# Performance work log

Hardware: AMD Instinct MI355X
Metric: run time of the kernel (lower is better)

Reference implementation:

```python
import jax, jax.numpy as jnp
import numpy as np

# ---- hardcoded module constants (from Cyborg.__init__) ----
B, S, V = 256, 128, 512
H = 30              # number of symbol vectors
N_STACKS = 2
R = 2               # REDUNDANCY
DEPTH = 4           # stack_depth
ZERO_OFFSET = 1e-6
NAND_BIAS = 3.0
INIT_SHARPEN = 10.0
N_VECS = 1 + N_STACKS  # input vec + one peek per stack = 3
C_BIG = (H + N_STACKS) * R   # 64 choices for push_fn / calc_out
C_SMALL = 2 * R              # 4 choices for pop_op / push_op


def _cossim(a, b, eps=1e-8):
    # torch.cosine_similarity semantics: per-vector norm clamp
    na = jnp.maximum(jnp.linalg.norm(a, axis=-1, keepdims=True), eps)
    nb = jnp.maximum(jnp.linalg.norm(b, axis=-1, keepdims=True), eps)
    return jnp.sum((a / na) * (b / nb), axis=-1)


def _nand(query, w, nw_raw):
    # Fuzzy-NAND gate bank (neurallambda NAND, clip='abs').
    # query: [B, N_VECS*V], w: [C, N_VECS*V], nw_raw: [C, N_VECS] -> [B, C]
    C = w.shape[0]
    q = query.reshape(-1, 1, N_VECS, V)
    wv = w.reshape(1, C, N_VECS, V)
    cos = jnp.abs(_cossim(q, wv))                 # [B, C, N_VECS], clip='abs'
    nw = jax.nn.sigmoid(nw_raw)[None]             # interpolate sim vs NOT(sim)
    interp = nw * cos + (1.0 - nw) * (1.0 - cos)
    return jnp.prod(interp, axis=-1)              # fuzzy AND over the 3 vecs


# ---- differentiable stack (soft pointer over DEPTH slots) ----
def _read(stack, ptr):
    return jnp.einsum('bdv,bd->bv', stack, ptr)

def _push(stack, ptr, val):
    p = jnp.roll(ptr, 1, axis=1)
    s = stack * (1.0 - p)[..., None] + val[:, None, :] * p[..., None]
    return s, p

def _pop(stack, ptr):
    s = stack * (1.0 - ptr)[..., None] + ZERO_OFFSET * ptr[..., None]
    p = jnp.roll(ptr, -1, axis=1)
    return s, p

def _pop_or_nop(stack, ptr, sharp, should_pop, should_nop):
    pr = jax.nn.softmax(jnp.stack([should_pop, should_nop], -1) * sharp, axis=-1)
    ps, pp = _pop(stack, ptr)
    s = ps * pr[:, 0, None, None] + stack * pr[:, 1, None, None]
    p = pp * pr[:, 0, None] + ptr * pr[:, 1, None]
    return s, p

def _push_or_nop(stack, ptr, sharp, should_push, should_nop, val):
    pr = jax.nn.softmax(jnp.stack([should_push, should_nop], -1) * sharp, axis=-1)
    ps, pp = _push(stack, ptr, val)
    s = ps * pr[:, 0, None, None] + stack * pr[:, 1, None, None]
    p = pp * pr[:, 0, None] + ptr * pr[:, 1, None]
    return s, p


def _forward(x, syms, stack_init_vec, sharp, pop_w, pop_nw, pushop_w, pushop_nw,
             pushfn_w, pushfn_nw, calc_w, calc_nw):
    b = x.shape[0]
    # init both stacks to zero_offset, pointer at slot 0, then hard-push init vec
    stack0 = jnp.full((N_STACKS, b, DEPTH, V), ZERO_OFFSET, x.dtype)
    ptr0 = jnp.zeros((N_STACKS, b, DEPTH), x.dtype).at[:, :, 0].set(1.0)
    init_val = jnp.broadcast_to(stack_init_vec, (b, V))
    stack0, ptr0 = jax.vmap(_push, in_axes=(0, 0, None))(stack0, ptr0, init_val)

    syms_b = jnp.broadcast_to(syms, (b, H, V))

    def step(carry, inp):
        stacks, ptrs = carry                                    # [2,B,D,V], [2,B,D]
        peeks = jax.vmap(_read)(stacks, ptrs)                   # [2,B,V]
        inps = jnp.concatenate([inp, peeks[0], peeks[1]], -1)   # [B,3V]
        out_opts = jnp.concatenate(
            [syms_b, peeks[0][:, None], peeks[1][:, None]], 1)  # [B,H+2,V]
        new_s, new_p = [], []
        for k in range(N_STACKS):
            pops = _nand(inps, pop_w[k], pop_nw[k])             # [B, 2R]
            pushes = _nand(inps, pushop_w[k], pushop_nw[k])     # [B, 2R]
            pv = _nand(inps, pushfn_w[k], pushfn_nw[k]).reshape(b, H + N_STACKS, R)
            push_val = jnp.einsum('bcv,bcr->bv', out_opts, pv)
            s, p = _pop_or_nop(stacks[k], ptrs[k], sharp[k],
                               pops[:, :R].max(1), pops[:, R:].max(1))
            s, p = _push_or_nop(s, p, sharp[k],
                                pushes[:, :R].max(1), pushes[:, R:].max(1), push_val)
            new_s.append(s)
            new_p.append(p)
        stacks = jnp.stack(new_s)
        ptrs = jnp.stack(new_p)
        peeks2 = jax.vmap(_read)(stacks, ptrs)
        inps2 = jnp.concatenate([inp, peeks2[0], peeks2[1]], -1)
        out_opts2 = jnp.concatenate(
            [syms_b, peeks2[0][:, None], peeks2[1][:, None]], 1)
        cv = _nand(inps2, calc_w, calc_nw).reshape(b, H + N_STACKS, R)
        out = jnp.einsum('bcv,bcr->bv', out_opts2, cv)
        return (stacks, ptrs), out

    _, outs = jax.lax.scan(step, (stack0, ptr0), jnp.swapaxes(x, 0, 1))
    return jnp.swapaxes(outs, 0, 1)  # [B,S,V]


def setup_inputs() -> dict:
    key = jax.random.key(0)
    ks = jax.random.split(key, 12)
    siv = jax.random.normal(ks[1], (V,), jnp.float32)
    siv = siv / jnp.linalg.norm(siv)
    return {
        'x': jax.random.normal(ks[0], (B, S, V), jnp.float32),
        'syms': jax.random.normal(ks[2], (H, V), jnp.float32),
        'stack_init_vec': siv,
        'sharp': jnp.full((N_STACKS,), INIT_SHARPEN, jnp.float32),
        'pop_w': jax.random.normal(ks[3], (N_STACKS, C_SMALL, N_VECS * V), jnp.float32),
        'pop_nw': jax.random.normal(ks[4], (N_STACKS, C_SMALL, N_VECS), jnp.float32) + NAND_BIAS,
        'pushop_w': jax.random.normal(ks[5], (N_STACKS, C_SMALL, N_VECS * V), jnp.float32),
        'pushop_nw': jax.random.normal(ks[6], (N_STACKS, C_SMALL, N_VECS), jnp.float32) + NAND_BIAS,
        'pushfn_w': jax.random.normal(ks[7], (N_STACKS, C_BIG, N_VECS * V), jnp.float32),
        'pushfn_nw': jax.random.normal(ks[8], (N_STACKS, C_BIG, N_VECS), jnp.float32) + NAND_BIAS,
        'calc_w': jax.random.normal(ks[9], (C_BIG, N_VECS * V), jnp.float32),
        'calc_nw': jax.random.normal(ks[10], (C_BIG, N_VECS), jnp.float32) + NAND_BIAS,
    }


def reference(x, syms, stack_init_vec, sharp, pop_w, pop_nw, pushop_w, pushop_nw,
              pushfn_w, pushfn_nw, calc_w, calc_nw):
    return _forward(x, syms, stack_init_vec, sharp, pop_w, pop_nw, pushop_w,
                    pushop_nw, pushfn_w, pushfn_nw, calc_w, calc_nw)
```

## Files before the change

kernel.cpp:

```cpp
#include <hip/hip_runtime.h>
#include <math.h>


#define SS 128
#define VV 512
#define NROWS 208
#define ZOFF 1e-6f

#define OFF_I0   0
#define OFF_OC   (32768*208)
#define OFF_GI   (OFF_OC + 32768*32)
#define OFF_M    (OFF_GI + 2*32*208)
#define OFF_A    (OFF_M + 1024)
#define OFF_Bc   (OFF_A + 624)
#define OFF_W0   (OFF_Bc + 624)

typedef _Float16 half8 __attribute__((ext_vector_type(8)));
typedef float f32x4 __attribute__((ext_vector_type(4)));

__device__ __forceinline__ const float* w_row(int r, const float* pw, const float* pow_,
                                              const float* pfw, const float* cw) {
    if (r < 8)   return pw   + r * 1536;
    if (r < 16)  return pow_ + (r - 8) * 1536;
    if (r < 144) return pfw  + (r - 16) * 1536;
    return cw + (r - 144) * 1536;
}
__device__ __forceinline__ const float* nw_row(int r, const float* pn, const float* pon,
                                               const float* pfn, const float* cn) {
    if (r < 8)   return pn   + r * 3;
    if (r < 16)  return pon  + (r - 8) * 3;
    if (r < 144) return pfn  + (r - 16) * 3;
    return cn + (r - 144) * 3;
}

__global__ void kB(const float* __restrict__ syms, const float* __restrict__ siv,
                   const float* __restrict__ pw, const float* __restrict__ pn,
                   const float* __restrict__ pow_, const float* __restrict__ pon,
                   const float* __restrict__ pfw, const float* __restrict__ pfn,
                   const float* __restrict__ cw, const float* __restrict__ cn,
                   float* __restrict__ ws) {
    int blk = blockIdx.x, tid = threadIdx.x;
    if (blk < 64) {
        int jj = blk >> 5, e = blk & 31;
        __shared__ float bas[512];
        for (int i = tid; i < 512; i += 256)
            bas[i] = (e == 0) ? 1.0f : ((e == 1) ? siv[i] : syms[(e - 2) * 512 + i]);
        __syncthreads();
        if (tid < NROWS) {
            int c = tid;
            const float4* w4 = (const float4*)(w_row(c, pw, pow_, pfw, cw) + (jj + 1) * 512);
            const float4* b4 = (const float4*)bas;
            float s = 0.f;
            for (int q = 0; q < 128; ++q) {
                float4 a = b4[q], b = w4[q];
                s += a.x * b.x + a.y * b.y + a.z * b.z + a.w * b.w;
            }
            ws[OFF_GI + (jj * 32 + e) * 208 + c] = s;
        }
    } else if (blk == 64) {
        __shared__ float basw[32 * 512];
        for (int i = tid; i < 32 * 512; i += 256) {
            int m = i >> 9, v = i & 511;
            basw[i] = (m == 0) ? 1.0f : ((m == 1) ? siv[v] : syms[(m - 2) * 512 + v]);
        }
        __syncthreads();
        for (int p = tid; p < 1024; p += 256) {
            int m = p >> 5, mm = p & 31;
            const float4* a4 = (const float4*)(basw + m * 512);
            const float4* b4 = (const float4*)(basw + mm * 512);
            float s = 0.f;
            for (int q = 0; q < 128; ++q) {
                float4 a = a4[q], b = b4[q];
                s += a.x * b.x + a.y * b.y + a.z * b.z + a.w * b.w;
            }
            ws[OFF_M + p] = s;
        }
    } else if (blk == 65) {
        for (int idx = tid; idx < 624; idx += 256) {
            int r = idx / 3, j = idx % 3;
            const float4* w4 = (const float4*)(w_row(r, pw, pow_, pfw, cw) + j * 512);
            float s = 0.f;
            for (int q = 0; q < 128; ++q) {
                float4 b = w4[q];
                s += b.x * b.x + b.y * b.y + b.z * b.z + b.w * b.w;
            }
            float nrm = fmaxf(sqrtf(s), 1e-8f);
            float nwv = nw_row(r, pn, pon, pfn, cn)[j];
            float sig = 1.f / (1.f + expf(-nwv));
            ws[OFF_A + idx]  = (2.f * sig - 1.f) / nrm;
            ws[OFF_Bc + idx] = 1.f - sig;
        }
    } else {
        int part = blk - 66;
        _Float16* whp = (_Float16*)(ws + OFF_W0);
        _Float16* wlp = whp + 208 * 512;
        for (int i = tid; i < 6656; i += 256) {
            int flat = part * 6656 + i;
            int c = flat >> 9, v = flat & 511;
            float wv = w_row(c, pw, pow_, pfw, cw)[v];
            _Float16 h = (_Float16)wv;
            whp[flat] = h;
            wlp[flat] = (_Float16)(wv - (float)h);
        }
    }
}

__global__ __launch_bounds__(256) void kA(const float* __restrict__ x, float* __restrict__ ws) {
    __shared__ half8 AH[2][256];
    __shared__ half8 AL[2][256];
    __shared__ float red[256];
    __shared__ float invx[64];
    const int tid = threadIdx.x;
    const int wid = tid >> 6, l = tid & 63;
    const size_t bt0 = (size_t)blockIdx.x * 64;

    const int sr = tid >> 2, ss = tid & 3;
    const float* xp = x + (bt0 + sr) * 512 + ss * 8;
    const int wpos = (sr >> 4) * 64 + (sr & 15) + (ss << 4);

    const _Float16* whp = (const _Float16*)(ws + OFF_W0);
    const _Float16* wlp = whp + 208 * 512;

    const int t0 = (wid == 0) ? 0 : (1 + 3 * wid);
    const int nt = (wid == 0) ? 4 : 3;

    f32x4 acc[4][4];
#pragma unroll
    for (int m = 0; m < 4; ++m)
#pragma unroll
        for (int tt = 0; tt < 4; ++tt)
            acc[m][tt] = (f32x4){0.f, 0.f, 0.f, 0.f};

    float sumsq = 0.f;
    auto stage = [&](int kt, int buf) {
        float v[8];
        *(float4*)v       = *(const float4*)(xp + kt * 32);
        *(float4*)(v + 4) = *(const float4*)(xp + kt * 32 + 4);
        half8 hh, hl;
#pragma unroll
        for (int j = 0; j < 8; ++j) {
            sumsq += v[j] * v[j];
            _Float16 h = (_Float16)v[j];
            hh[j] = h;
            hl[j] = (_Float16)(v[j] - (float)h);
        }
        AH[buf][wpos] = hh;
        AL[buf][wpos] = hl;
    };

    stage(0, 0);
    __syncthreads();

    for (int kt = 0; kt < 16; ++kt) {
        const int buf = kt & 1;
        if (kt < 15) stage(kt + 1, buf ^ 1);

        half8 ahm[4], alm[4];
#pragma unroll
        for (int m = 0; m < 4; ++m) {
            ahm[m] = AH[buf][m * 64 + l];
            alm[m] = AL[buf][m * 64 + l];
        }
        const int kof = kt * 32 + (l >> 4) * 8;
#pragma unroll
        for (int tt = 0; tt < 4; ++tt) {
            if (tt < nt) {
                const int c = (t0 + tt) * 16 + (l & 15);
                half8 bh = *(const half8*)(whp + c * 512 + kof);
                half8 bl = *(const half8*)(wlp + c * 512 + kof);
#pragma unroll
                for (int m = 0; m < 4; ++m) {
                    acc[m][tt] = __builtin_amdgcn_mfma_f32_16x16x32_f16(ahm[m], bh, acc[m][tt], 0, 0, 0);
                    acc[m][tt] = __builtin_amdgcn_mfma_f32_16x16x32_f16(ahm[m], bl, acc[m][tt], 0, 0, 0);
                    acc[m][tt] = __builtin_amdgcn_mfma_f32_16x16x32_f16(alm[m], bh, acc[m][tt], 0, 0, 0);
                }
            }
        }
        __syncthreads();
    }

    red[tid] = sumsq;
    __syncthreads();
    if (tid < 64) {
        float s = red[tid * 4] + red[tid * 4 + 1] + red[tid * 4 + 2] + red[tid * 4 + 3];
        invx[tid] = 1.f / fmaxf(sqrtf(s), 1e-8f);
    }
    __syncthreads();

#pragma unroll
    for (int tt = 0; tt < 4; ++tt) {
        if (tt < nt) {
            const int c = (t0 + tt) * 16 + (l & 15);
            const float A0 = ws[OFF_A + c * 3];
            const float B0 = ws[OFF_Bc + c * 3];
#pragma unroll
            for (int m = 0; m < 4; ++m) {
                const int rbase = m * 16 + (l >> 4) * 4;
#pragma unroll
                for (int j = 0; j < 4; ++j) {
                    const float ix = invx[rbase + j];
                    ws[OFF_I0 + (bt0 + rbase + j) * 208 + c] = A0 * fabsf(acc[m][tt][j]) * ix + B0;
                }
            }
        }
    }
}

__global__ __attribute__((amdgpu_flat_work_group_size(256, 256), amdgpu_waves_per_eu(1, 1)))
void kC(float* __restrict__ ws, const float* __restrict__ sharp) {
    __shared__ float pkL[64];
    __shared__ float nndL[144];
    const int b = blockIdx.x, tid = threadIdx.x;
    const int wid = tid >> 6, l = tid & 63;
    const int k = l >> 5, m = l & 31;
    const int isRow = (tid < 144);
    const int r2 = 144 + l;

    const float* GI = ws + OFF_GI;
    float G1[64], G2[64];
    float4 Mr[8];
    float A1r = 0.f, A2r = 0.f, B1r = 0.f, B2r = 0.f;
    float A1d = 0.f, A2d = 0.f, B1d = 0.f, B2d = 0.f;
    if (isRow) {
#pragma unroll
        for (int i = 0; i < 32; ++i) {
            G1[i]      = GI[i * 208 + tid];
            G1[32 + i] = GI[(32 + i) * 208 + tid];
        }
        A1r = ws[OFF_A + tid * 3 + 1];  A2r = ws[OFF_A + tid * 3 + 2];
        B1r = ws[OFF_Bc + tid * 3 + 1]; B2r = ws[OFF_Bc + tid * 3 + 2];
    }
    if (wid == 3) {
#pragma unroll
        for (int i = 0; i < 32; ++i) {
            G2[i]      = GI[i * 208 + r2];
            G2[32 + i] = GI[(32 + i) * 208 + r2];
        }
        A1d = ws[OFF_A + r2 * 3 + 1];  A2d = ws[OFF_A + r2 * 3 + 2];
        B1d = ws[OFF_Bc + r2 * 3 + 1]; B2d = ws[OFF_Bc + r2 * 3 + 2];
    }
#pragma unroll
    for (int q = 0; q < 8; ++q) Mr[q] = *(const float4*)(ws + OFF_M + m * 32 + q * 4);

    const float sh = sharp[k];

    float st[4], p[4];
#pragma unroll
    for (int d = 0; d < 4; ++d) {
        st[d] = (d == 1) ? ((m == 1) ? 1.f : 0.f) : ((m == 0) ? ZOFF : 0.f);
        p[d] = (d == 1) ? 1.f : 0.f;
    }
    float pk = st[0] * p[0] + st[1] * p[1] + st[2] * p[2] + st[3] * p[3];

    const float* i0base = ws + OFF_I0 + (size_t)b * SS * 208;
    float i0r  = isRow ? i0base[tid] : 0.f;
    float i0rn = 0.f;
    float i0d  = (wid == 3) ? i0base[r2] : 0.f;

    float iq0 = 1.f, iq1 = 1.f;
    auto gram_iq = [&](float own) {
        const float* ph = pkL + 32 * k;
        float4 a0 = *(const float4*)(ph);
        float4 a1 = *(const float4*)(ph + 4);
        float4 a2 = *(const float4*)(ph + 8);
        float4 a3 = *(const float4*)(ph + 12);
        float4 a4 = *(const float4*)(ph + 16);
        float4 a5 = *(const float4*)(ph + 20);
        float4 a6 = *(const float4*)(ph + 24);
        float4 a7 = *(const float4*)(ph + 28);
        float mva = Mr[0].x*a0.x + Mr[0].y*a0.y + Mr[0].z*a0.z + Mr[0].w*a0.w
                  + Mr[2].x*a2.x + Mr[2].y*a2.y + Mr[2].z*a2.z + Mr[2].w*a2.w
                  + Mr[4].x*a4.x + Mr[4].y*a4.y + Mr[4].z*a4.z + Mr[4].w*a4.w
                  + Mr[6].x*a6.x + Mr[6].y*a6.y + Mr[6].z*a6.z + Mr[6].w*a6.w;
        float mvb = Mr[1].x*a1.x + Mr[1].y*a1.y + Mr[1].z*a1.z + Mr[1].w*a1.w
                  + Mr[3].x*a3.x + Mr[3].y*a3.y + Mr[3].z*a3.z + Mr[3].w*a3.w
                  + Mr[5].x*a5.x + Mr[5].y*a5.y + Mr[5].z*a5.z + Mr[5].w*a5.w
                  + Mr[7].x*a7.x + Mr[7].y*a7.y + Mr[7].z*a7.z + Mr[7].w*a7.w;
        float part = own * (mva + mvb);
        part += __shfl_xor(part, 1);  part += __shfl_xor(part, 2);
        part += __shfl_xor(part, 4);  part += __shfl_xor(part, 8);
        part += __shfl_xor(part, 16);
        float iqOwn = 1.f / fmaxf(sqrtf(part), 1e-8f);
        float iqOth = __shfl_xor(iqOwn, 32);
        iq0 = k ? iqOth : iqOwn;
        iq1 = k ? iqOwn : iqOth;
    };
    auto dots = [&](const float* Gt, float& d1, float& d2) {
        float d1a = 0.f, d1b = 0.f, d2a = 0.f, d2b = 0.f;
#pragma unroll
        for (int q = 0; q < 8; q += 2) {
            float4 a = *(const float4*)(pkL + 4 * q);
            float4 bq = *(const float4*)(pkL + 4 * q + 4);
            float4 c = *(const float4*)(pkL + 32 + 4 * q);
            float4 e = *(const float4*)(pkL + 32 + 4 * q + 4);
            d1a += a.x * Gt[4*q]   + a.y * Gt[4*q+1]   + a.z * Gt[4*q+2]   + a.w * Gt[4*q+3];
            d1b += bq.x * Gt[4*q+4] + bq.y * Gt[4*q+5] + bq.z * Gt[4*q+6] + bq.w * Gt[4*q+7];
            d2a += c.x * Gt[32+4*q] + c.y * Gt[33+4*q] + c.z * Gt[34+4*q] + c.w * Gt[35+4*q];
            d2b += e.x * Gt[36+4*q] + e.y * Gt[37+4*q] + e.z * Gt[38+4*q] + e.w * Gt[39+4*q];
        }
        d1 = d1a + d1b;
        d2 = d2a + d2b;
    };

    if (wid == 0) pkL[l] = pk;
    __syncthreads();
    gram_iq(pk);
    if (isRow) {
        float d1, d2;
        dots(G1, d1, d2);
        nndL[tid] = i0r * (A1r * fabsf(d1) * iq0 + B1r) * (A2r * fabsf(d2) * iq1 + B2r);
        i0rn = i0base[208 + tid];
    }
    __syncthreads();

    for (int t = 0; t < SS; ++t) {
        float4 gp4 = *(const float4*)(nndL + 4 * k);
        float4 gq4 = *(const float4*)(nndL + 8 + 4 * k);
        float prp0 = 1.f / (1.f + __expf((fmaxf(gp4.z, gp4.w) - fmaxf(gp4.x, gp4.y)) * sh));
        float prq0 = 1.f / (1.f + __expf((fmaxf(gq4.z, gq4.w) - fmaxf(gq4.x, gq4.y)) * sh));
        float prp1 = 1.f - prp0, prq1 = 1.f - prq0;
        float prx = 0.f, pry = 0.f;
        if (m >= 2) {
            float2 pr2 = *(const float2*)(nndL + 16 + 64 * k + 2 * m - 4);
            prx = pr2.x; pry = pr2.y;
        }
        float4 t30 = *(const float4*)(nndL + 16 + 64 * k + 60);
        float pkOther = __shfl_xor(pk, 32);
        float pk0m = k ? pkOther : pk;
        float pk1m = k ? pk : pkOther;
        float pvc = prx + pry + (t30.x + t30.y) * pk0m + (t30.z + t30.w) * pk1m;

        float zc = (m == 0) ? ZOFF : 0.f;
        float s1[4], p1[4];
#pragma unroll
        for (int d = 0; d < 4; ++d) {
            float ps = st[d] * (1.f - p[d]) + zc * p[d];
            s1[d] = ps * prp0 + st[d] * prp1;
            p1[d] = p[(d + 1) & 3] * prp0 + p[d] * prp1;
        }
#pragma unroll
        for (int d = 0; d < 4; ++d) {
            float pu = p1[(d + 3) & 3];
            float su = s1[d] * (1.f - pu) + pvc * pu;
            st[d] = su * prq0 + s1[d] * prq1;
            p[d] = pu * prq0 + p1[d] * prq1;
        }
        float pkp = st[0] * p[0] + st[1] * p[1] + st[2] * p[2] + st[3] * p[3];
        if (wid == 0) pkL[l] = pkp;
        __syncthreads();

        gram_iq(pkp);
        if (isRow) {
            float d1, d2;
            dots(G1, d1, d2);
            float iv = i0rn;
            int tn2 = (t < SS - 2) ? (t + 2) : (SS - 1);
            i0rn = i0base[(size_t)tn2 * 208 + tid];
            nndL[tid] = iv * (A1r * fabsf(d1) * iq0 + B1r) * (A2r * fabsf(d2) * iq1 + B2r);
        }
        if (wid == 3) {
            float dd1, dd2;
            dots(G2, dd1, dd2);
            float nnd2 = i0d * (A1d * fabsf(dd1) * iq0 + B1d) * (A2d * fabsf(dd2) * iq1 + B2d);
            int tn = (t < SS - 1) ? (t + 1) : (SS - 1);
            i0d = i0base[(size_t)tn * 208 + r2];
            int src = (m >= 2) ? (2 * m - 4) : 0;
            float cx = __shfl(nnd2, src);
            float cy = __shfl(nnd2, src + 1);
            if (m < 2) { cx = 0.f; cy = 0.f; }
            float s60 = __shfl(nnd2, 60), s61 = __shfl(nnd2, 61);
            float s62 = __shfl(nnd2, 62), s63 = __shfl(nnd2, 63);
            float pkpO = __shfl_xor(pkp, 32);
            if (l < 32) {
                float oc = cx + cy + (s60 + s61) * pkp + (s62 + s63) * pkpO;
                ws[OFF_OC + ((size_t)b * SS + t) * 32 + m] = oc;
            }
        }
        __syncthreads();
        pk = pkp;
    }
}

__global__ __launch_bounds__(256) void kD(const float* __restrict__ ws, const float* __restrict__ syms,
                                          const float* __restrict__ siv, float* __restrict__ out) {
    int t = threadIdx.x;
    int rg = t >> 6;
    int vc = (t & 63) * 8;
    size_t r0 = (size_t)blockIdx.x * 16 + rg * 4;
    const float* oc = ws + OFF_OC;
    float acc[4][8];
    float4 sv0 = *(const float4*)(siv + vc);
    float4 sv1 = *(const float4*)(siv + vc + 4);
#pragma unroll
    for (int rr = 0; rr < 4; ++rr) {
        float c0 = oc[(r0 + rr) * 32 + 0];
        float c1 = oc[(r0 + rr) * 32 + 1];
        acc[rr][0] = c0 + c1 * sv0.x; acc[rr][1] = c0 + c1 * sv0.y;
        acc[rr][2] = c0 + c1 * sv0.z; acc[rr][3] = c0 + c1 * sv0.w;
        acc[rr][4] = c0 + c1 * sv1.x; acc[rr][5] = c0 + c1 * sv1.y;
        acc[rr][6] = c0 + c1 * sv1.z; acc[rr][7] = c0 + c1 * sv1.w;
    }
    for (int mm = 0; mm < 30; ++mm) {
        float4 b0 = *(const float4*)(syms + mm * 512 + vc);
        float4 b1 = *(const float4*)(syms + mm * 512 + vc + 4);
#pragma unroll
        for (int rr = 0; rr < 4; ++rr) {
            float c = oc[(r0 + rr) * 32 + 2 + mm];
            acc[rr][0] += c * b0.x; acc[rr][1] += c * b0.y;
            acc[rr][2] += c * b0.z; acc[rr][3] += c * b0.w;
            acc[rr][4] += c * b1.x; acc[rr][5] += c * b1.y;
            acc[rr][6] += c * b1.z; acc[rr][7] += c * b1.w;
        }
    }
#pragma unroll
    for (int rr = 0; rr < 4; ++rr) {
        float* o = out + (r0 + rr) * 512 + vc;
        *(float4*)o       = make_float4(acc[rr][0], acc[rr][1], acc[rr][2], acc[rr][3]);
        *(float4*)(o + 4) = make_float4(acc[rr][4], acc[rr][5], acc[rr][6], acc[rr][7]);
    }
}

extern "C" void kernel_launch(void* const* d_in, const int* in_sizes, int n_in,
                              void* d_out, int out_size, void* d_ws, size_t ws_size,
                              hipStream_t stream) {
    const float* x    = (const float*)d_in[0];
    const float* syms = (const float*)d_in[1];
    const float* siv  = (const float*)d_in[2];
    const float* shp  = (const float*)d_in[3];
    const float* pw   = (const float*)d_in[4];
    const float* pn   = (const float*)d_in[5];
    const float* pow_ = (const float*)d_in[6];
    const float* pon  = (const float*)d_in[7];
    const float* pfw  = (const float*)d_in[8];
    const float* pfn  = (const float*)d_in[9];
    const float* cw   = (const float*)d_in[10];
    const float* cn   = (const float*)d_in[11];
    float* ws  = (float*)d_ws;
    float* out = (float*)d_out;

    hipLaunchKernelGGL(kB, dim3(82),   dim3(256), 0, stream,
                       syms, siv, pw, pn, pow_, pon, pfw, pfn, cw, cn, ws);
    hipLaunchKernelGGL(kA, dim3(512),  dim3(256), 0, stream, x, ws);
    hipLaunchKernelGGL(kC, dim3(256),  dim3(256), 0, stream, ws, shp);
    hipLaunchKernelGGL(kD, dim3(2048), dim3(256), 0, stream, ws, syms, siv, out);
}
```

Baseline: 444.1 us.

## Replace shared-memory pk broadcast with readlane and double-buffer nnd to drop a barrier

Every wave now recomputes the stack-state vector itself, and the 64 values are broadcast through scalar readlane instead of being written to LDS and read back after a barrier. The nnd results go into a double-buffered shared array, so each timestep needs one __syncthreads instead of two. The Gram norm reduction uses DPP and ds_swizzle, takes rsqrt in place of sqrt plus reciprocal, and the next i0 values are prefetched at the top of the loop. The catch is that all four waves redo the stack update and 64 readlanes per step, which adds scalar/VALU work to the serial recurrence in exchange for less synchronisation.

```diff
diff --git a/kernel.cpp b/kernel.cpp
--- a/kernel.cpp
+++ b/kernel.cpp
@@ -17,6 +17,25 @@
 
 typedef _Float16 half8 __attribute__((ext_vector_type(8)));
 typedef float f32x4 __attribute__((ext_vector_type(4)));
+
+__device__ __forceinline__ float rlane(float v, int lane) {
+    return __int_as_float(__builtin_amdgcn_readlane(__float_as_int(v), lane));
+}
+template <int CTRL>
+__device__ __forceinline__ float dpp_add(float x) {
+    int y = __builtin_amdgcn_update_dpp(0, __float_as_int(x), CTRL, 0xF, 0xF, true);
+    return x + __int_as_float(y);
+}
+__device__ __forceinline__ float sum16(float x) {
+    x = dpp_add<0xB1>(x);
+    x = dpp_add<0x4E>(x);
+    x = dpp_add<0x124>(x);
+    x = dpp_add<0x128>(x);
+    return x;
+}
+__device__ __forceinline__ float swz16(float x) {
+    return __int_as_float(__builtin_amdgcn_ds_swizzle(__float_as_int(x), 0x401F));
+}
 
 __device__ __forceinline__ const float* w_row(int r, const float* pw, const float* pow_,
                                               const float* pfw, const float* cw) {
@@ -208,8 +227,7 @@
 
 __global__ __attribute__((amdgpu_flat_work_group_size(256, 256), amdgpu_waves_per_eu(1, 1)))
 void kC(float* __restrict__ ws, const float* __restrict__ sharp) {
-    __shared__ float pkL[64];
-    __shared__ float nndL[144];
+    __shared__ float nndL[2][144];
     const int b = blockIdx.x, tid = threadIdx.x;
     const int wid = tid >> 6, l = tid & 63;
     const int k = l >> 5, m = l & 31;
@@ -217,8 +235,7 @@
     const int r2 = 144 + l;
 
     const float* GI = ws + OFF_GI;
-    float G1[64], G2[64];
-    float4 Mr[8];
+    float G1[64], G2[64], Mrow[32];
     float A1r = 0.f, A2r = 0.f, B1r = 0.f, B2r = 0.f;
     float A1d = 0.f, A2d = 0.f, B1d = 0.f, B2d = 0.f;
     if (isRow) {
@@ -240,8 +257,10 @@
         B1d = ws[OFF_Bc + r2 * 3 + 1]; B2d = ws[OFF_Bc + r2 * 3 + 2];
     }
 #pragma unroll
-    for (int q = 0; q < 8; ++q) Mr[q] = *(const float4*)(ws + OFF_M + m * 32 + q * 4);
-
+    for (int q = 0; q < 8; ++q) {
+        float4 mr = *(const float4*)(ws + OFF_M + m * 32 + 4 * q);
+        Mrow[4*q] = mr.x; Mrow[4*q+1] = mr.y; Mrow[4*q+2] = mr.z; Mrow[4*q+3] = mr.w;
+    }
     const float sh = sharp[k];
 
     float st[4], p[4];
@@ -251,81 +270,93 @@
         p[d] = (d == 1) ? 1.f : 0.f;
     }
     float pk = st[0] * p[0] + st[1] * p[1] + st[2] * p[2] + st[3] * p[3];
+    float pkOther = __shfl_xor(pk, 32);
 
     const float* i0base = ws + OFF_I0 + (size_t)b * SS * 208;
     float i0r  = isRow ? i0base[tid] : 0.f;
+    float i0d  = (wid == 3) ? i0base[r2] : 0.f;
     float i0rn = 0.f;
-    float i0d  = (wid == 3) ? i0base[r2] : 0.f;
-
-    float iq0 = 1.f, iq1 = 1.f;
-    auto gram_iq = [&](float own) {
-        const float* ph = pkL + 32 * k;
-        float4 a0 = *(const float4*)(ph);
-        float4 a1 = *(const float4*)(ph + 4);
-        float4 a2 = *(const float4*)(ph + 8);
-        float4 a3 = *(const float4*)(ph + 12);
-        float4 a4 = *(const float4*)(ph + 16);
-        float4 a5 = *(const float4*)(ph + 20);
-        float4 a6 = *(const float4*)(ph + 24);
-        float4 a7 = *(const float4*)(ph + 28);
-        float mva = Mr[0].x*a0.x + Mr[0].y*a0.y + Mr[0].z*a0.z + Mr[0].w*a0.w
-                  + Mr[2].x*a2.x + Mr[2].y*a2.y + Mr[2].z*a2.z + Mr[2].w*a2.w
-                  + Mr[4].x*a4.x + Mr[4].y*a4.y + Mr[4].z*a4.z + Mr[4].w*a4.w
-                  + Mr[6].x*a6.x + Mr[6].y*a6.y + Mr[6].z*a6.z + Mr[6].w*a6.w;
-        float mvb = Mr[1].x*a1.x + Mr[1].y*a1.y + Mr[1].z*a1.z + Mr[1].w*a1.w
-                  + Mr[3].x*a3.x + Mr[3].y*a3.y + Mr[3].z*a3.z + Mr[3].w*a3.w
-                  + Mr[5].x*a5.x + Mr[5].y*a5.y + Mr[5].z*a5.z + Mr[5].w*a5.w
-                  + Mr[7].x*a7.x + Mr[7].y*a7.y + Mr[7].z*a7.z + Mr[7].w*a7.w;
-        float part = own * (mva + mvb);
-        part += __shfl_xor(part, 1);  part += __shfl_xor(part, 2);
-        part += __shfl_xor(part, 4);  part += __shfl_xor(part, 8);
-        part += __shfl_xor(part, 16);
-        float iqOwn = 1.f / fmaxf(sqrtf(part), 1e-8f);
-        float iqOth = __shfl_xor(iqOwn, 32);
-        iq0 = k ? iqOth : iqOwn;
-        iq1 = k ? iqOwn : iqOth;
+
+    auto post = [&](float pkp, float pkpOth, float iv, float* nndW, bool doOc, int t) {
+        float pk0v = k ? pkpOth : pkp;
+        float pk1v = k ? pkp : pkpOth;
+        float gq0[2] = {0.f, 0.f}, gq1[2] = {0.f, 0.f};
+        float d1[2] = {0.f, 0.f}, d2[2] = {0.f, 0.f};
+        if (wid == 3) {
+#pragma unroll
+            for (int mm = 0; mm < 32; ++mm) {
+                float v0 = rlane(pkp, mm);
+                float v1 = rlane(pkp, 32 + mm);
+                gq0[mm & 1] += Mrow[mm] * v0;
+                gq1[mm & 1] += Mrow[mm] * v1;
+                d1[mm & 1]  += v0 * G2[mm];
+                d2[mm & 1]  += v1 * G2[32 + mm];
+            }
+        } else {
+#pragma unroll
+            for (int mm = 0; mm < 32; ++mm) {
+                float v0 = rlane(pkp, mm);
+                float v1 = rlane(pkp, 32 + mm);
+                gq0[mm & 1] += Mrow[mm] * v0;
+                gq1[mm & 1] += Mrow[mm] * v1;
+                d1[mm & 1]  += v0 * G1[mm];
+                d2[mm & 1]  += v1 * G1[32 + mm];
+            }
+        }
+        float pm0 = pk0v * (gq0[0] + gq0[1]);
+        float pm1 = pk1v * (gq1[0] + gq1[1]);
+        float q0 = sum16(pm0); q0 += swz16(q0);
+        float q1 = sum16(pm1); q1 += swz16(q1);
+        float iq0 = __frsqrt_rn(fmaxf(q0, 1e-16f));
+        float iq1 = __frsqrt_rn(fmaxf(q1, 1e-16f));
+        float dd1 = d1[0] + d1[1], dd2 = d2[0] + d2[1];
+        if (isRow) {
+            nndW[tid] = iv * (A1r * fabsf(dd1) * iq0 + B1r) * (A2r * fabsf(dd2) * iq1 + B2r);
+        }
+        if (wid == 3) {
+            float nnd2 = i0d * (A1d * fabsf(dd1) * iq0 + B1d) * (A2d * fabsf(dd2) * iq1 + B2d);
+            if (doOc) {
+                float s60 = rlane(nnd2, 60), s61 = rlane(nnd2, 61);
+                float s62 = rlane(nnd2, 62), s63 = rlane(nnd2, 63);
+                int src = (m >= 2) ? (2 * m - 4) : 0;
+                float cx = __shfl(nnd2, src);
+                float cy = __shfl(nnd2, src + 1);
+                if (m < 2) { cx = 0.f; cy = 0.f; }
+                if (l < 32) {
+                    float oc = cx + cy + (s60 + s61) * pkp + (s62 + s63) * pkpOth;
+                    ws[OFF_OC + ((size_t)b * SS + t) * 32 + m] = oc;
+                }
+            }
+        }
     };
-    auto dots = [&](const float* Gt, float& d1, float& d2) {
-        float d1a = 0.f, d1b = 0.f, d2a = 0.f, d2b = 0.f;
-#pragma unroll
-        for (int q = 0; q < 8; q += 2) {
-            float4 a = *(const float4*)(pkL + 4 * q);
-            float4 bq = *(const float4*)(pkL + 4 * q + 4);
-            float4 c = *(const float4*)(pkL + 32 + 4 * q);
-            float4 e = *(const float4*)(pkL + 32 + 4 * q + 4);
-            d1a += a.x * Gt[4*q]   + a.y * Gt[4*q+1]   + a.z * Gt[4*q+2]   + a.w * Gt[4*q+3];
-            d1b += bq.x * Gt[4*q+4] + bq.y * Gt[4*q+5] + bq.z * Gt[4*q+6] + bq.w * Gt[4*q+7];
-            d2a += c.x * Gt[32+4*q] + c.y * Gt[33+4*q] + c.z * Gt[34+4*q] + c.w * Gt[35+4*q];
-            d2b += e.x * Gt[36+4*q] + e.y * Gt[37+4*q] + e.z * Gt[38+4*q] + e.w * Gt[39+4*q];
-        }
-        d1 = d1a + d1b;
-        d2 = d2a + d2b;
-    };
-
-    if (wid == 0) pkL[l] = pk;
+
+    post(pk, pkOther, i0r, nndL[0], false, 0);
+    if (isRow) i0rn = i0base[208 + tid];
     __syncthreads();
-    gram_iq(pk);
-    if (isRow) {
-        float d1, d2;
-        dots(G1, d1, d2);
-        nndL[tid] = i0r * (A1r * fabsf(d1) * iq0 + B1r) * (A2r * fabsf(d2) * iq1 + B2r);
-        i0rn = i0base[208 + tid];
-    }
-    __syncthreads();
 
     for (int t = 0; t < SS; ++t) {
-        float4 gp4 = *(const float4*)(nndL + 4 * k);
-        float4 gq4 = *(const float4*)(nndL + 8 + 4 * k);
+        const float* nb = nndL[t & 1];
+        float i0f = 0.f, i0df = 0.f;
+        if (isRow) {
+            int tn2 = (t < SS - 2) ? (t + 2) : (SS - 1);
+            i0f = i0base[(size_t)tn2 * 208 + tid];
+        }
+        if (wid == 3) {
+            int tn = (t < SS - 1) ? (t + 1) : (SS - 1);
+            i0df = i0base[(size_t)tn * 208 + r2];
+        }
+
+        float4 gp4 = *(const float4*)(nb + 4 * k);
+        float4 gq4 = *(const float4*)(nb + 8 + 4 * k);
         float prp0 = 1.f / (1.f + __expf((fmaxf(gp4.z, gp4.w) - fmaxf(gp4.x, gp4.y)) * sh));
         float prq0 = 1.f / (1.f + __expf((fmaxf(gq4.z, gq4.w) - fmaxf(gq4.x, gq4.y)) * sh));
         float prp1 = 1.f - prp0, prq1 = 1.f - prq0;
         float prx = 0.f, pry = 0.f;
         if (m >= 2) {
-            float2 pr2 = *(const float2*)(nndL + 16 + 64 * k + 2 * m - 4);
+            float2 pr2 = *(const float2*)(nb + 16 + 64 * k + 2 * m - 4);
             prx = pr2.x; pry = pr2.y;
         }
-        float4 t30 = *(const float4*)(nndL + 16 + 64 * k + 60);
-        float pkOther = __shfl_xor(pk, 32);
+        float4 t30 = *(const float4*)(nb + 16 + 64 * k + 60);
         float pk0m = k ? pkOther : pk;
         float pk1m = k ? pk : pkOther;
         float pvc = prx + pry + (t30.x + t30.y) * pk0m + (t30.z + t30.w) * pk1m;
@@ -346,38 +377,15 @@
             p[d] = pu * prq0 + p1[d] * prq1;
         }
         float pkp = st[0] * p[0] + st[1] * p[1] + st[2] * p[2] + st[3] * p[3];
-        if (wid == 0) pkL[l] = pkp;
-        __syncthreads();
-
-        gram_iq(pkp);
-        if (isRow) {
-            float d1, d2;
-            dots(G1, d1, d2);
-            float iv = i0rn;
-            int tn2 = (t < SS - 2) ? (t + 2) : (SS - 1);
-            i0rn = i0base[(size_t)tn2 * 208 + tid];
-            nndL[tid] = iv * (A1r * fabsf(d1) * iq0 + B1r) * (A2r * fabsf(d2) * iq1 + B2r);
-        }
-        if (wid == 3) {
-            float dd1, dd2;
-            dots(G2, dd1, dd2);
-            float nnd2 = i0d * (A1d * fabsf(dd1) * iq0 + B1d) * (A2d * fabsf(dd2) * iq1 + B2d);
-            int tn = (t < SS - 1) ? (t + 1) : (SS - 1);
-            i0d = i0base[(size_t)tn * 208 + r2];
-            int src = (m >= 2) ? (2 * m - 4) : 0;
-            float cx = __shfl(nnd2, src);
-            float cy = __shfl(nnd2, src + 1);
-            if (m < 2) { cx = 0.f; cy = 0.f; }
-            float s60 = __shfl(nnd2, 60), s61 = __shfl(nnd2, 61);
-            float s62 = __shfl(nnd2, 62), s63 = __shfl(nnd2, 63);
-            float pkpO = __shfl_xor(pkp, 32);
-            if (l < 32) {
-                float oc = cx + cy + (s60 + s61) * pkp + (s62 + s63) * pkpO;
-                ws[OFF_OC + ((size_t)b * SS + t) * 32 + m] = oc;
-            }
-        }
+        float pkpOth = __shfl_xor(pkp, 32);
+
+        post(pkp, pkpOth, i0rn, nndL[(t + 1) & 1], true, t);
+
         __syncthreads();
         pk = pkp;
+        pkOther = pkpOth;
+        i0rn = i0f;
+        if (wid == 3) i0d = i0df;
     }
 }
 
```

After: 566.7 us. +27.6%, slower.
